# Kernel optimization log

Measured on AMD Instinct MI355X. Metric: run time of the kernel, lower is better.

Reference implementation:

```python
import jax, jax.numpy as jnp
import numpy as np

N_Q = 6        # qubits per circuit
N_CL = 32      # entangler layers per circuit
N_MOD = 32     # number of qlayer modules (feature parts)
PART = 64      # 2048 // 32

# Pauli-Z sign table: state flattened as (B, 2**N_Q) with wire 0 the most
# significant axis; signs[k, i] = (-1)**bit_i(k).
_bits = (np.arange(2 ** N_Q)[:, None] >> np.arange(N_Q - 1, -1, -1)[None, :]) & 1
SIGNS = jnp.asarray(1.0 - 2.0 * _bits, dtype=jnp.float32)  # [64, 6]


def _apply_1q(state, gate, wire):
    # state: [B, 2, 2, 2, 2, 2, 2] complex64; gate: [2, 2]
    axis = 1 + wire
    state = jnp.tensordot(gate, state, axes=((1,), (axis,)))
    return jnp.moveaxis(state, 0, axis)


def _apply_cnot(state, ctrl, tgt):
    ci, ti = 1 + ctrl, 1 + tgt
    s0 = jax.lax.index_in_dim(state, 0, ci, keepdims=True)
    s1 = jax.lax.index_in_dim(state, 1, ci, keepdims=True)
    return jnp.concatenate([s0, jnp.flip(s1, axis=ti)], axis=ci)


def _rx(theta):
    c = jnp.cos(theta * 0.5).astype(jnp.complex64)
    s = jnp.sin(theta * 0.5).astype(jnp.complex64)
    return jnp.stack([jnp.stack([c, -1j * s]), jnp.stack([-1j * s, c])])


def _circuit(angles, weights):
    # angles: [B, 6] (AngleEmbedding RY params); weights: [N_CL, 6] (RX params)
    B = angles.shape[0]
    half = angles * 0.5
    # RY(a)|0> = cos(a/2)|0> + sin(a/2)|1>  -> product state
    amps = jnp.stack([jnp.cos(half), jnp.sin(half)], axis=-1).astype(jnp.complex64)  # [B,6,2]
    state = amps[:, 0]
    for q in range(1, N_Q):
        state = state[..., None] * amps[:, q].reshape((B,) + (1,) * q + (2,))
    # state: [B,2,2,2,2,2,2]

    def layer(st, w):
        # BasicEntanglerLayers: RX on every wire, then ring of CNOTs
        for q in range(N_Q):
            st = _apply_1q(st, _rx(w[q]), q)
        for q in range(N_Q):
            st = _apply_cnot(st, q, (q + 1) % N_Q)
        return st, None

    state, _ = jax.lax.scan(jax.checkpoint(layer), state, weights)
    probs = (state.real ** 2 + state.imag ** 2).reshape(B, 2 ** N_Q)
    return probs @ SIGNS  # [B, 6] expvals of PauliZ on each wire


def _forward(features, Wp, bp, qw, Wf, bf):
    B = features.shape[0]
    parts = features.reshape(B, N_MOD, PART)                 # 32 chunks of 64
    angles = jnp.einsum('bpd,qd->bpq', parts, Wp) + bp       # shared projector -> [B,32,6]
    outs = jax.vmap(_circuit, in_axes=(1, 0), out_axes=1)(angles, qw)  # [B,32,6]
    return outs.reshape(B, N_MOD * N_Q) @ Wf.T + bf          # [B, num_classes]


def setup_inputs() -> dict:
    key = jax.random.key(0)
    k1, k2, k3, k4 = jax.random.split(key, 4)
    B, num_classes = 2048, 150
    features = jax.random.normal(k1, (B, 2048), dtype=jnp.float32)
    Wp = jax.random.normal(k2, (N_Q, PART), dtype=jnp.float32) * (1.0 / np.sqrt(PART))
    bp = jnp.zeros((N_Q,), dtype=jnp.float32)
    qw = jax.random.uniform(k3, (N_MOD, N_CL, N_Q), dtype=jnp.float32) * (2.0 * np.pi)
    Wf = jax.random.normal(k4, (num_classes, N_MOD * N_Q), dtype=jnp.float32) * (1.0 / np.sqrt(N_MOD * N_Q))
    bf = jnp.zeros((num_classes,), dtype=jnp.float32)
    return {'features': features, 'Wp': Wp, 'bp': bp, 'qw': qw, 'Wf': Wf, 'bf': bf}


def reference(features, Wp, bp, qw, Wf, bf):
    return _forward(features, Wp, bp, qw, Wf, bf)
```

## Files before the change

### kernel.cpp

```cpp
#include <hip/hip_runtime.h>

#define NQ   6
#define DIM  64
#define NMOD 32
#define NCL  32
#define BATCH 2048
#define NCLS 150
#define KF   192
#define NROWS (BATCH*NMOD)

#define OFF_UT    0
#define OFF_CAMPS 262144
#define OFF_OUTS  1048576

__global__ __launch_bounds__(192) void k_angles(const float* __restrict__ features,
                                                const float* __restrict__ Wp,
                                                const float* __restrict__ bp,
                                                float* __restrict__ camps) {
    __shared__ float ldsA[64 * 33];
    __shared__ float ldsW[NQ * 64];
    int tid = threadIdx.x;
    int rowbase = blockIdx.x * 32;
    const float* src = features + (size_t)rowbase * 64;
    for (int idx = tid; idx < 32 * 64; idx += 192) {
        int r = idx >> 6, d = idx & 63;
        ldsA[d * 33 + r] = src[idx];
    }
    for (int idx = tid; idx < NQ * 64; idx += 192) ldsW[idx] = Wp[idx];
    __syncthreads();

    int q = tid >> 5;
    int r = tid & 31;
    float acc = 0.f;
#pragma unroll
    for (int d = 0; d < 64; ++d) acc += ldsA[d * 33 + r] * ldsW[q * 64 + d];
    float half = 0.5f * (acc + bp[q]);
    float s, c;
    sincosf(half, &s, &c);
    int row = rowbase + r;
    camps[(row * NQ + q) * 2 + 0] = c;
    camps[(row * NQ + q) * 2 + 1] = s;
}

__global__ __launch_bounds__(256) void k_prep(const float* __restrict__ qw,
                                              float* __restrict__ UTf) {
    __shared__ float2 csl[NCL * NQ];
    int tid = threadIdx.x;
    int lane = tid & 63;
    int w = tid >> 6;
    int p = blockIdx.x >> 4;
    int col = ((blockIdx.x & 15) << 2) + w;

    if (tid < NCL * NQ) {
        float s, c;
        sincosf(0.5f * qw[p * NCL * NQ + tid], &s, &c);
        csl[tid] = make_float2(c, s);
    }
    __syncthreads();

    int dst = lane;
#pragma unroll
    for (int q = 0; q < NQ; ++q) {
        int cm = 1 << (5 - q), tm = 1 << (5 - ((q + 1) % 6));
        dst ^= (dst & cm) ? tm : 0;
    }
    int dst_b = dst << 2;

    float re = (lane == col) ? 1.f : 0.f;
    float im = 0.f;

    for (int layer = 0; layer < NCL; ++layer) {
#pragma unroll
        for (int q = 0; q < NQ; ++q) {
            float2 cs = csl[layer * NQ + q];
            int mask = 1 << (5 - q);
            float pre = __shfl_xor(re, mask, 64);
            float pim = __shfl_xor(im, mask, 64);
            float nre = fmaf(cs.x, re, cs.y * pim);
            float nim = fmaf(cs.x, im, -cs.y * pre);
            re = nre;
            im = nim;
        }
        re = __int_as_float(__builtin_amdgcn_ds_permute(dst_b, __float_as_int(re)));
        im = __int_as_float(__builtin_amdgcn_ds_permute(dst_b, __float_as_int(im)));
    }
    float2* UT2 = (float2*)UTf;
    UT2[p * (DIM * DIM) + lane * DIM + col] = make_float2(re, im);
}

__global__ __launch_bounds__(256, 4) void k_circuit(const float* __restrict__ camps,
                                                    const float* __restrict__ UTf,
                                                    float* __restrict__ outs) {
    __shared__ float zl[4][5][64];
    int tid = threadIdx.x;
    int lane = tid & 63;
    int w = tid >> 6;
    int wq = __builtin_amdgcn_readfirstlane(w);
    int p = blockIdx.x & 31;
    int btile = blockIdx.x >> 5;
    int b = btile * 64 + lane;

    float ca[12];
    {
        const float4* cp = (const float4*)(camps + (size_t)(b * NMOD + p) * NQ * 2);
        float4 c0 = cp[0], c1 = cp[1], c2 = cp[2];
        ca[0] = c0.x; ca[1] = c0.y; ca[2] = c0.z; ca[3] = c0.w;
        ca[4] = c1.x; ca[5] = c1.y; ca[6] = c1.z; ca[7] = c1.w;
        ca[8] = c2.x; ca[9] = c2.y; ca[10] = c2.z; ca[11] = c2.w;
    }

    float psi[DIM];
    psi[0] = 1.f;
#pragma unroll
    for (int q = 5; q >= 0; --q) {
        int sz = 1 << (5 - q);
        float c = ca[2 * q], s = ca[2 * q + 1];
#pragma unroll
        for (int k = 0; k < 64; ++k) {
            if (k < sz) {
                psi[k + sz] = psi[k] * s;
                psi[k] = psi[k] * c;
            }
        }
    }

    float ps = 0.f, z2 = 0.f, z3 = 0.f, z4 = 0.f, z5 = 0.f;
    const float4* Ubase = (const float4*)(UTf + (size_t)p * DIM * DIM * 2);

#pragma unroll
    for (int ii = 0; ii < 16; ++ii) {
        int i = wq * 16 + ii;
        const float4* Ur = Ubase + i * 32;
        float yre = 0.f, yim = 0.f;
#pragma unroll
        for (int j4 = 0; j4 < 32; ++j4) {
            float4 u = Ur[j4];
            yre = fmaf(u.x, psi[2 * j4], yre);
            yim = fmaf(u.y, psi[2 * j4], yim);
            yre = fmaf(u.z, psi[2 * j4 + 1], yre);
            yim = fmaf(u.w, psi[2 * j4 + 1], yim);
        }
        float prob = fmaf(yre, yre, yim * yim);
        ps += prob;
        z2 += (ii & 8) ? -prob : prob;
        z3 += (ii & 4) ? -prob : prob;
        z4 += (ii & 2) ? -prob : prob;
        z5 += (ii & 1) ? -prob : prob;
    }

    zl[w][0][lane] = ps;
    zl[w][1][lane] = z2;
    zl[w][2][lane] = z3;
    zl[w][3][lane] = z4;
    zl[w][4][lane] = z5;
    __syncthreads();

    if (tid < 64) {
        float p0 = zl[0][0][tid], p1 = zl[1][0][tid], p2 = zl[2][0][tid], p3 = zl[3][0][tid];
        float z0 = (p0 + p1) - (p2 + p3);
        float z1 = (p0 - p1) + (p2 - p3);
        float o2 = zl[0][1][tid] + zl[1][1][tid] + zl[2][1][tid] + zl[3][1][tid];
        float o3 = zl[0][2][tid] + zl[1][2][tid] + zl[2][2][tid] + zl[3][2][tid];
        float o4 = zl[0][3][tid] + zl[1][3][tid] + zl[2][3][tid] + zl[3][3][tid];
        float o5 = zl[0][4][tid] + zl[1][4][tid] + zl[2][4][tid] + zl[3][4][tid];
        int bb = btile * 64 + tid;
        float* o = outs + (size_t)bb * KF + p * NQ;
        o[0] = z0; o[1] = z1; o[2] = o2; o[3] = o3; o[4] = o4; o[5] = o5;
    }
}

__global__ __launch_bounds__(256) void k_final(const float* __restrict__ outs,
                                               const float* __restrict__ Wf,
                                               const float* __restrict__ bf,
                                               float* __restrict__ out) {
    int tid = threadIdx.x;
    int b = blockIdx.x * 64 + (tid & 63);
    int c = blockIdx.y * 4 + (tid >> 6);
    if (c >= NCLS) return;
    float acc = bf[c];
    const float* orow = outs + (size_t)b * KF;
    const float* wrow = Wf + (size_t)c * KF;
#pragma unroll
    for (int k = 0; k < KF; k += 4) {
        float4 o = *(const float4*)&orow[k];
        float4 wv = *(const float4*)&wrow[k];
        acc = fmaf(o.x, wv.x, acc);
        acc = fmaf(o.y, wv.y, acc);
        acc = fmaf(o.z, wv.z, acc);
        acc = fmaf(o.w, wv.w, acc);
    }
    out[b * NCLS + c] = acc;
}

extern "C" void kernel_launch(void* const* d_in, const int* in_sizes, int n_in,
                              void* d_out, int out_size, void* d_ws, size_t ws_size,
                              hipStream_t stream) {
    const float* features = (const float*)d_in[0];
    const float* Wp       = (const float*)d_in[1];
    const float* bp       = (const float*)d_in[2];
    const float* qw       = (const float*)d_in[3];
    const float* Wf       = (const float*)d_in[4];
    const float* bf       = (const float*)d_in[5];
    float* out = (float*)d_out;
    float* ws  = (float*)d_ws;

    float* UT    = ws + OFF_UT;
    float* camps = ws + OFF_CAMPS;
    float* outsb = ws + OFF_OUTS;

    k_angles<<<NROWS / 32, 192, 0, stream>>>(features, Wp, bp, camps);
    k_prep<<<NMOD * 16, 256, 0, stream>>>(qw, UT);
    k_circuit<<<NMOD * (BATCH / 64), 256, 0, stream>>>(camps, UT, outsb);
    k_final<<<dim3(BATCH / 64, (NCLS + 3) / 4), 256, 0, stream>>>(outsb, Wf, bf, out);
}
```

Before: 164.2 us.

## Fuse angle projection into circuit kernel via shared-memory staging

Removes the separate angle kernel and computes the 64-wide projection, bias and sincos inside the circuit kernel. Each block loads its 64-row by 64-feature tile into padded LDS, computes the six angles per row, and stores cos/sin to LDS for the state preparation. This cuts one launch and the global round trip of the camps buffer. In exchange the circuit kernel uses more LDS, which may reduce occupancy, and gains two extra barriers.

```diff
diff --git a/kernel.cpp b/kernel.cpp
--- a/kernel.cpp
+++ b/kernel.cpp
@@ -10,37 +10,7 @@
 #define NROWS (BATCH*NMOD)
 
 #define OFF_UT    0
-#define OFF_CAMPS 262144
-#define OFF_OUTS  1048576
-
-__global__ __launch_bounds__(192) void k_angles(const float* __restrict__ features,
-                                                const float* __restrict__ Wp,
-                                                const float* __restrict__ bp,
-                                                float* __restrict__ camps) {
-    __shared__ float ldsA[64 * 33];
-    __shared__ float ldsW[NQ * 64];
-    int tid = threadIdx.x;
-    int rowbase = blockIdx.x * 32;
-    const float* src = features + (size_t)rowbase * 64;
-    for (int idx = tid; idx < 32 * 64; idx += 192) {
-        int r = idx >> 6, d = idx & 63;
-        ldsA[d * 33 + r] = src[idx];
-    }
-    for (int idx = tid; idx < NQ * 64; idx += 192) ldsW[idx] = Wp[idx];
-    __syncthreads();
-
-    int q = tid >> 5;
-    int r = tid & 31;
-    float acc = 0.f;
-#pragma unroll
-    for (int d = 0; d < 64; ++d) acc += ldsA[d * 33 + r] * ldsW[q * 64 + d];
-    float half = 0.5f * (acc + bp[q]);
-    float s, c;
-    sincosf(half, &s, &c);
-    int row = rowbase + r;
-    camps[(row * NQ + q) * 2 + 0] = c;
-    camps[(row * NQ + q) * 2 + 1] = s;
-}
+#define OFF_OUTS  262144
 
 __global__ __launch_bounds__(256) void k_prep(const float* __restrict__ qw,
                                               float* __restrict__ UTf) {
@@ -88,26 +58,68 @@
     UT2[p * (DIM * DIM) + lane * DIM + col] = make_float2(re, im);
 }
 
-__global__ __launch_bounds__(256, 4) void k_circuit(const float* __restrict__ camps,
-                                                    const float* __restrict__ UTf,
-                                                    float* __restrict__ outs) {
+__global__ __launch_bounds__(256, 4) void k_fused(const float* __restrict__ features,
+                                                  const float* __restrict__ Wp,
+                                                  const float* __restrict__ bp,
+                                                  const float* __restrict__ UTf,
+                                                  float* __restrict__ outs) {
+    __shared__ float ldsA[64 * 65];
+    __shared__ float ldsW[NQ * 64];
+    __shared__ float camps_l[64 * 13];
     __shared__ float zl[4][5][64];
+
     int tid = threadIdx.x;
     int lane = tid & 63;
     int w = tid >> 6;
     int wq = __builtin_amdgcn_readfirstlane(w);
     int p = blockIdx.x & 31;
     int btile = blockIdx.x >> 5;
-    int b = btile * 64 + lane;
+
+    {
+        int l = tid >> 2;
+        int quarter = tid & 3;
+        const float* src = features + (size_t)(btile * 64 + l) * 2048 + p * 64
+                         + quarter * 16;
+        float4 v0 = *(const float4*)(src + 0);
+        float4 v1 = *(const float4*)(src + 4);
+        float4 v2 = *(const float4*)(src + 8);
+        float4 v3 = *(const float4*)(src + 12);
+        int d0 = quarter * 16;
+        float tmp[16] = {v0.x,v0.y,v0.z,v0.w, v1.x,v1.y,v1.z,v1.w,
+                         v2.x,v2.y,v2.z,v2.w, v3.x,v3.y,v3.z,v3.w};
+#pragma unroll
+        for (int j = 0; j < 16; ++j) ldsA[(d0 + j) * 65 + l] = tmp[j];
+        for (int idx = tid; idx < NQ * 64; idx += 256) ldsW[idx] = Wp[idx];
+    }
+    __syncthreads();
+
+    {
+        int l = tid & 63;
+        int q0 = tid >> 6;
+        float acc0 = 0.f, acc1 = 0.f;
+        bool two = (q0 < 2);
+        int q1 = q0 + 4;
+#pragma unroll
+        for (int d = 0; d < 64; ++d) {
+            float a = ldsA[d * 65 + l];
+            acc0 = fmaf(a, ldsW[q0 * 64 + d], acc0);
+            if (two) acc1 = fmaf(a, ldsW[q1 * 64 + d], acc1);
+        }
+        float s, c;
+        sincosf(0.5f * (acc0 + bp[q0]), &s, &c);
+        camps_l[l * 13 + 2 * q0 + 0] = c;
+        camps_l[l * 13 + 2 * q0 + 1] = s;
+        if (two) {
+            sincosf(0.5f * (acc1 + bp[q1]), &s, &c);
+            camps_l[l * 13 + 2 * q1 + 0] = c;
+            camps_l[l * 13 + 2 * q1 + 1] = s;
+        }
+    }
+    __syncthreads();
 
     float ca[12];
-    {
-        const float4* cp = (const float4*)(camps + (size_t)(b * NMOD + p) * NQ * 2);
-        float4 c0 = cp[0], c1 = cp[1], c2 = cp[2];
-        ca[0] = c0.x; ca[1] = c0.y; ca[2] = c0.z; ca[3] = c0.w;
-        ca[4] = c1.x; ca[5] = c1.y; ca[6] = c1.z; ca[7] = c1.w;
-        ca[8] = c2.x; ca[9] = c2.y; ca[10] = c2.z; ca[11] = c2.w;
-    }
+#pragma unroll
+    for (int j = 0; j < 12; ++j) ca[j] = camps_l[lane * 13 + j];
 
     float psi[DIM];
     psi[0] = 1.f;
@@ -205,11 +217,9 @@
     float* ws  = (float*)d_ws;
 
     float* UT    = ws + OFF_UT;
-    float* camps = ws + OFF_CAMPS;
     float* outsb = ws + OFF_OUTS;
 
-    k_angles<<<NROWS / 32, 192, 0, stream>>>(features, Wp, bp, camps);
     k_prep<<<NMOD * 16, 256, 0, stream>>>(qw, UT);
-    k_circuit<<<NMOD * (BATCH / 64), 256, 0, stream>>>(camps, UT, outsb);
+    k_fused<<<NMOD * (BATCH / 64), 256, 0, stream>>>(features, Wp, bp, UT, outsb);
     k_final<<<dim3(BATCH / 64, (NCLS + 3) / 4), 256, 0, stream>>>(outsb, Wf, bf, out);
 }
```

Result: no change. 164.2 us (-0.0%).
